# Optimization experiments

Hardware: AMD Instinct MI355X
Metric: run time of the kernel (lower is better)

The kernel has to match this reference:

```python
import jax, jax.numpy as jnp
import numpy as np

D_MODEL = 1024
D_STATE = 8
EXPAND = 2
EPS = 1e-5


def setup_inputs() -> dict:
    key = jax.random.key(0)
    ks = jax.random.split(key, 8)
    d_inner = D_MODEL * EXPAND
    x = jax.random.normal(ks[0], (2, 128, 196, D_MODEL), dtype=jnp.float32)
    # Linear params (torch convention: W [out, in], y = x @ W.T + b)
    W_proj = jax.random.normal(ks[1], (d_inner, D_MODEL), dtype=jnp.float32) * (1.0 / np.sqrt(D_MODEL))
    b_proj = jnp.zeros((d_inner,), dtype=jnp.float32)
    W_state = jax.random.normal(ks[2], (D_STATE, d_inner), dtype=jnp.float32) * (1.0 / np.sqrt(d_inner))
    b_state = jnp.zeros((D_STATE,), dtype=jnp.float32)
    W_out = jax.random.normal(ks[3], (D_MODEL, D_STATE), dtype=jnp.float32) * (1.0 / np.sqrt(D_STATE))
    b_out = jnp.zeros((D_MODEL,), dtype=jnp.float32)
    initial_state = jnp.zeros((1, D_STATE), dtype=jnp.float32)
    gamma = jnp.ones((D_MODEL,), dtype=jnp.float32)
    beta = jnp.zeros((D_MODEL,), dtype=jnp.float32)
    return {
        "x": x,
        "W_proj": W_proj, "b_proj": b_proj,
        "W_state": W_state, "b_state": b_state,
        "W_out": W_out, "b_out": b_out,
        "initial_state": initial_state,
        "gamma": gamma, "beta": beta,
    }


def reference(x, W_proj, b_proj, W_state, b_state, W_out, b_out, initial_state, gamma, beta):
    # The torch module loops over seq_len, but every step reads the fixed
    # initial_state (no recurrence) -> fully vectorized over all dims.
    # LayerNorm over d_model (eps=1e-5, torch default)
    mu = jnp.mean(x, axis=-1, keepdims=True)
    var = jnp.mean(jnp.square(x - mu), axis=-1, keepdims=True)
    xn = (x - mu) * jax.lax.rsqrt(var + EPS) * gamma + beta
    # proj: [b, s, p, d_model] -> [b, s, p, d_inner], then SiLU
    proj = jax.nn.silu(jnp.einsum('bspd,ed->bspe', xn, W_proj) + b_proj)
    # state projection: -> [b, s, p, d_state]
    state_updates = jnp.einsum('bspe,ne->bspn', proj, W_state) + b_state
    # initial_state [1, d_state] broadcast-added, then SiLU
    current_state = jax.nn.silu(initial_state.reshape(1, 1, 1, D_STATE) + state_updates)
    # out projection: -> [b, s, p, d_model]; dropout=0 (eval mode)
    out = jnp.einsum('bspn,dn->bspd', current_state, W_out) + b_out
    return x + out
```

## Files before the change

kernel.cpp:

```cpp
#include <hip/hip_runtime.h>
#include <hip/hip_bf16.h>

typedef unsigned short u16;
typedef unsigned int u32;
typedef __attribute__((ext_vector_type(8))) short bf16x8;
typedef __attribute__((ext_vector_type(4))) short bf16x4;
typedef __attribute__((ext_vector_type(4))) float f32x4;

#define T_TOKENS 50176
#define D_MODEL  1024
#define D_INNER  2048
#define D_STATE  8

__device__ __forceinline__ u16 f2bf(float f) {
    u32 u = __builtin_bit_cast(u32, f);
    u += 0x7fffu + ((u >> 16) & 1u);
    return (u16)(u >> 16);
}
__device__ __forceinline__ float bf2f(u16 h) {
    u32 u = ((u32)h) << 16;
    return __builtin_bit_cast(float, u);
}
__device__ __forceinline__ float silu(float v) {
    return v / (1.f + __expf(-v));
}

__device__ __forceinline__ f32x4 mfma_16x16x16_bf16(bf16x4 a, bf16x4 b, f32x4 c) {
#if __has_builtin(__builtin_amdgcn_mfma_f32_16x16x16bf16_1k)
    return __builtin_amdgcn_mfma_f32_16x16x16bf16_1k(a, b, c, 0, 0, 0);
#else
    f32x4 d;
    asm("v_mfma_f32_16x16x16_bf16 %0, %1, %2, %3" : "=v"(d) : "v"(a), "v"(b), "v"(c));
    return d;
#endif
}

__global__ __launch_bounds__(256) void k_ln(const float* __restrict__ x,
                                            const float* __restrict__ gamma,
                                            const float* __restrict__ beta,
                                            u16* __restrict__ xn) {
    const int w = threadIdx.x >> 6, lane = threadIdx.x & 63;
    const int tok = blockIdx.x * 4 + w;
    const float* xr = x + (size_t)tok * D_MODEL;
    float4 v[4];
    float s1 = 0.f, s2 = 0.f;
#pragma unroll
    for (int c = 0; c < 4; ++c) {
        v[c] = *(const float4*)(xr + c * 256 + lane * 4);
        s1 += v[c].x + v[c].y + v[c].z + v[c].w;
        s2 += v[c].x * v[c].x + v[c].y * v[c].y + v[c].z * v[c].z + v[c].w * v[c].w;
    }
#pragma unroll
    for (int off = 32; off; off >>= 1) {
        s1 += __shfl_xor(s1, off, 64);
        s2 += __shfl_xor(s2, off, 64);
    }
    const float mu = s1 * (1.f / 1024.f);
    const float var = s2 * (1.f / 1024.f) - mu * mu;
    const float rstd = rsqrtf(var + 1e-5f);
    u16* orow = xn + (size_t)tok * D_MODEL;
#pragma unroll
    for (int c = 0; c < 4; ++c) {
        const int d = c * 256 + lane * 4;
        float4 g = *(const float4*)(gamma + d);
        float4 b = *(const float4*)(beta + d);
        ushort4 o;
        o.x = f2bf((v[c].x - mu) * rstd * g.x + b.x);
        o.y = f2bf((v[c].y - mu) * rstd * g.y + b.y);
        o.z = f2bf((v[c].z - mu) * rstd * g.z + b.z);
        o.w = f2bf((v[c].w - mu) * rstd * g.w + b.w);
        *(ushort4*)(orow + d) = o;
    }
}

__global__ __launch_bounds__(256) void k_cvt(const float* __restrict__ W, u16* __restrict__ Wb) {
    const int i = (blockIdx.x * 256 + threadIdx.x) * 4;
    float4 v = *(const float4*)(W + i);
    ushort4 o = {f2bf(v.x), f2bf(v.y), f2bf(v.z), f2bf(v.w)};
    *(ushort4*)(Wb + i) = o;
}

__global__ __launch_bounds__(256) void k_gemm(const u16* __restrict__ A,
                                              const u16* __restrict__ B,
                                              const float* __restrict__ bproj,
                                              const float* __restrict__ Wstate,
                                              float* __restrict__ part) {
    __shared__ u16 As[128 * 64];
    __shared__ u16 Bs[128 * 64];
    const int t = threadIdx.x;
    const int w = t >> 6, lane = t & 63;
    const int q = lane >> 4, c15 = lane & 15;
    const int bn = blockIdx.x, bm = blockIdx.y;
    const int wm = (w >> 1) * 64, wn = (w & 1) * 64;

    f32x4 acc[4][4];
#pragma unroll
    for (int ci = 0; ci < 4; ++ci)
#pragma unroll
        for (int ti = 0; ti < 4; ++ti) acc[ci][ti] = (f32x4){0.f, 0.f, 0.f, 0.f};

    const int srow = t >> 3;
    const int sch = (t & 7) ^ (srow & 7);
    const u16* Ag = A + (size_t)(bm * 128 + srow) * 1024 + sch * 8;
    const u16* Bg = B + (size_t)(bn * 128 + srow) * 1024 + sch * 8;
    u16* lA = &As[t * 8];
    u16* lB = &Bs[t * 8];

    for (int kb = 0; kb < 16; ++kb) {
        __syncthreads();
#pragma unroll
        for (int i = 0; i < 4; ++i) {
            __builtin_amdgcn_global_load_lds(
                (const __attribute__((address_space(1))) void*)(Ag + (size_t)i * 32 * 1024 + kb * 64),
                (__attribute__((address_space(3))) void*)(lA + i * 2048), 16, 0, 0);
            __builtin_amdgcn_global_load_lds(
                (const __attribute__((address_space(1))) void*)(Bg + (size_t)i * 32 * 1024 + kb * 64),
                (__attribute__((address_space(3))) void*)(lB + i * 2048), 16, 0, 0);
        }
        __syncthreads();
#pragma unroll
        for (int ks = 0; ks < 2; ++ks) {
            bf16x8 xf[4], wf[4];
            const int chb = (ks * 4 + q) ^ (c15 & 7);
#pragma unroll
            for (int ti = 0; ti < 4; ++ti)
                xf[ti] = *(const bf16x8*)&As[(wm + ti * 16 + c15) * 64 + chb * 8];
#pragma unroll
            for (int ci = 0; ci < 4; ++ci)
                wf[ci] = *(const bf16x8*)&Bs[(wn + ci * 16 + c15) * 64 + chb * 8];
#pragma unroll
            for (int ci = 0; ci < 4; ++ci)
#pragma unroll
                for (int ti = 0; ti < 4; ++ti)
                    acc[ci][ti] = __builtin_amdgcn_mfma_f32_16x16x32_bf16(wf[ci], xf[ti], acc[ci][ti], 0, 0, 0);
        }
    }

    const int ib0 = bn * 128 + wn + q * 4;
    f32x4 bp4[4];
    bf16x4 wsf[4];
#pragma unroll
    for (int ci = 0; ci < 4; ++ci) {
        const int ib = ib0 + ci * 16;
        bp4[ci] = *(const f32x4*)(bproj + ib);
        if (c15 < 8) {
            f32x4 wv = *(const f32x4*)(Wstate + (size_t)c15 * D_INNER + ib);
            wsf[ci] = (bf16x4){(short)f2bf(wv[0]), (short)f2bf(wv[1]), (short)f2bf(wv[2]), (short)f2bf(wv[3])};
        } else {
            wsf[ci] = (bf16x4){0, 0, 0, 0};
        }
    }
    const int slot = bn * 2 + (w & 1);
#pragma unroll
    for (int ti = 0; ti < 4; ++ti) {
        f32x4 a2 = (f32x4){0.f, 0.f, 0.f, 0.f};
#pragma unroll
        for (int ci = 0; ci < 4; ++ci) {
            bf16x4 sv;
#pragma unroll
            for (int r = 0; r < 4; ++r) {
                const float s = silu(acc[ci][ti][r] + bp4[ci][r]);
                sv[r] = (short)f2bf(s);
            }
            a2 = mfma_16x16x16_bf16(wsf[ci], sv, a2);
        }
        if (q < 2) {
            const int row = bm * 128 + wm + ti * 16 + c15;
            *(f32x4*)(part + (size_t)row * 256 + slot * 8 + q * 4) = a2;
        }
    }
}

__global__ __launch_bounds__(256) void k_out2(const float* __restrict__ x,
                                              const float* __restrict__ part,
                                              const float* __restrict__ Wout,
                                              const float* __restrict__ bout,
                                              const float* __restrict__ bstate,
                                              const float* __restrict__ s0,
                                              float* __restrict__ out) {
    __shared__ float4 wol[2048];
    const int t = threadIdx.x;
    const float4* Wg4 = (const float4*)Wout;
#pragma unroll
    for (int i = 0; i < 8; ++i) {
        const int g = i * 256 + t;
        const int d = g >> 1;
        wol[g ^ ((d >> 2) & 7)] = Wg4[g];
    }
    __syncthreads();

    const int w = t >> 6, lane = t & 63;
    const int tok = blockIdx.x * 4 + w;

    const float4* p4 = (const float4*)(part + (size_t)tok * 256);
    float4 pv = p4[lane];
    float pa[4] = {pv.x, pv.y, pv.z, pv.w};
#pragma unroll
    for (int off = 2; off < 64; off <<= 1)
#pragma unroll
        for (int j = 0; j < 4; ++j) pa[j] += __shfl_xor(pa[j], off, 64);
    float cs[8];
#pragma unroll
    for (int j = 0; j < 4; ++j) {
        const float sl = __shfl(pa[j], 0, 64);
        const float sh = __shfl(pa[j], 1, 64);
        cs[j]     = silu(sl + s0[j]     + bstate[j]);
        cs[4 + j] = silu(sh + s0[4 + j] + bstate[4 + j]);
    }

    const float* xr = x + (size_t)tok * D_MODEL;
    float* orow = out + (size_t)tok * D_MODEL;
#pragma unroll
    for (int c = 0; c < 16; ++c) {
        const int d = c * 64 + lane;
        const int m = (d >> 2) & 7;
        const float4 w0 = wol[(d * 2) ^ m];
        const float4 w1 = wol[(d * 2 + 1) ^ m];
        float a = xr[d] + bout[d];
        a += cs[0] * w0.x + cs[1] * w0.y + cs[2] * w0.z + cs[3] * w0.w;
        a += cs[4] * w1.x + cs[5] * w1.y + cs[6] * w1.z + cs[7] * w1.w;
        orow[d] = a;
    }
}

extern "C" void kernel_launch(void* const* d_in, const int* in_sizes, int n_in,
                              void* d_out, int out_size, void* d_ws, size_t ws_size,
                              hipStream_t stream) {
    const float* x      = (const float*)d_in[0];
    const float* Wproj  = (const float*)d_in[1];
    const float* bproj  = (const float*)d_in[2];
    const float* Wstate = (const float*)d_in[3];
    const float* bstate = (const float*)d_in[4];
    const float* Wout   = (const float*)d_in[5];
    const float* bout   = (const float*)d_in[6];
    const float* s0     = (const float*)d_in[7];
    const float* gamma  = (const float*)d_in[8];
    const float* beta   = (const float*)d_in[9];

    u16* xn = (u16*)d_out;
    u16* Wb = (u16*)d_ws;
    float* partials = (float*)((char*)d_ws + (size_t)D_INNER * D_MODEL * sizeof(u16));
    float* out = (float*)d_out;

    k_ln  <<<T_TOKENS / 4, 256, 0, stream>>>(x, gamma, beta, xn);
    k_cvt <<<(D_INNER * D_MODEL) / 1024, 256, 0, stream>>>(Wproj, Wb);
    k_gemm<<<dim3(D_INNER / 128, T_TOKENS / 128), 256, 0, stream>>>(xn, Wb, bproj, Wstate, partials);
    k_out2<<<T_TOKENS / 4, 256, 0, stream>>>(x, partials, Wout, bout, bstate, s0, out);
}
```

Measured before the change: 745.3 us.

## Enlarge GEMM tile to 256x256 with double-buffered LDS pipeline

Result: faster. 692.6 us (-7.1%).

```diff
diff --git a/kernel.cpp b/kernel.cpp
--- a/kernel.cpp
+++ b/kernel.cpp
@@ -16,10 +16,6 @@
     u32 u = __builtin_bit_cast(u32, f);
     u += 0x7fffu + ((u >> 16) & 1u);
     return (u16)(u >> 16);
-}
-__device__ __forceinline__ float bf2f(u16 h) {
-    u32 u = ((u32)h) << 16;
-    return __builtin_bit_cast(float, u);
 }
 __device__ __forceinline__ float silu(float v) {
     return v / (1.f + __expf(-v));
@@ -80,63 +76,132 @@
     *(ushort4*)(Wb + i) = o;
 }
 
-__global__ __launch_bounds__(256) void k_gemm(const u16* __restrict__ A,
-                                              const u16* __restrict__ B,
-                                              const float* __restrict__ bproj,
-                                              const float* __restrict__ Wstate,
-                                              float* __restrict__ part) {
-    __shared__ u16 As[128 * 64];
-    __shared__ u16 Bs[128 * 64];
+#define STAGE_A(i, kb, buf) \
+    __builtin_amdgcn_global_load_lds( \
+        (const __attribute__((address_space(1))) void*)(Ag + (i) * 65536 + (kb) * 64), \
+        (__attribute__((address_space(3))) void*)(lA + (buf) * 32768 + (i) * 4096), 16, 0, 0)
+#define STAGE_B(i, kb, buf) \
+    __builtin_amdgcn_global_load_lds( \
+        (const __attribute__((address_space(1))) void*)(Bg + (i) * 65536 + (kb) * 64), \
+        (__attribute__((address_space(3))) void*)(lB + (buf) * 32768 + (i) * 4096), 16, 0, 0)
+#define FENCE() asm volatile("" ::: "memory")
+#define BARRIER() do { FENCE(); __builtin_amdgcn_s_barrier(); FENCE(); } while (0)
+
+__global__ __launch_bounds__(512, 2) void k_gemm(const u16* __restrict__ A,
+                                                 const u16* __restrict__ B,
+                                                 const float* __restrict__ bproj,
+                                                 const float* __restrict__ Wstate,
+                                                 float* __restrict__ part) {
+    __shared__ u16 sm[65536];
     const int t = threadIdx.x;
     const int w = t >> 6, lane = t & 63;
     const int q = lane >> 4, c15 = lane & 15;
     const int bn = blockIdx.x, bm = blockIdx.y;
-    const int wm = (w >> 1) * 64, wn = (w & 1) * 64;
-
-    f32x4 acc[4][4];
+    const int wm = (w >> 2) * 128, wn = (w & 3) * 64;
+
+    f32x4 acc[4][8];
 #pragma unroll
     for (int ci = 0; ci < 4; ++ci)
 #pragma unroll
-        for (int ti = 0; ti < 4; ++ti) acc[ci][ti] = (f32x4){0.f, 0.f, 0.f, 0.f};
+        for (int ti = 0; ti < 8; ++ti) acc[ci][ti] = (f32x4){0.f, 0.f, 0.f, 0.f};
 
     const int srow = t >> 3;
-    const int sch = (t & 7) ^ (srow & 7);
-    const u16* Ag = A + (size_t)(bm * 128 + srow) * 1024 + sch * 8;
-    const u16* Bg = B + (size_t)(bn * 128 + srow) * 1024 + sch * 8;
-    u16* lA = &As[t * 8];
-    u16* lB = &Bs[t * 8];
-
-    for (int kb = 0; kb < 16; ++kb) {
-        __syncthreads();
-#pragma unroll
-        for (int i = 0; i < 4; ++i) {
-            __builtin_amdgcn_global_load_lds(
-                (const __attribute__((address_space(1))) void*)(Ag + (size_t)i * 32 * 1024 + kb * 64),
-                (__attribute__((address_space(3))) void*)(lA + i * 2048), 16, 0, 0);
-            __builtin_amdgcn_global_load_lds(
-                (const __attribute__((address_space(1))) void*)(Bg + (size_t)i * 32 * 1024 + kb * 64),
-                (__attribute__((address_space(3))) void*)(lB + i * 2048), 16, 0, 0);
-        }
-        __syncthreads();
-#pragma unroll
-        for (int ks = 0; ks < 2; ++ks) {
-            bf16x8 xf[4], wf[4];
-            const int chb = (ks * 4 + q) ^ (c15 & 7);
+    const int gch = (t & 7) ^ (srow & 7);
+    const u16* Ag = A + (size_t)(bm * 256 + srow) * 1024 + gch * 8;
+    const u16* Bg = B + (size_t)(bn * 256 + srow) * 1024 + gch * 8;
+    u16* lA = &sm[t * 8];
+    u16* lB = &sm[16384 + t * 8];
+
+    auto LDA = [&](int buf, int ti, int ks) -> bf16x8 {
+        const int row = wm + ti * 16 + c15;
+        const int ch = (ks * 4 + q) ^ (c15 & 7);
+        return *(const bf16x8*)&sm[buf * 32768 + row * 64 + ch * 8];
+    };
+    auto LDB = [&](int buf, int ci, int ks) -> bf16x8 {
+        const int row = wn + ci * 16 + c15;
+        const int ch = (ks * 4 + q) ^ (c15 & 7);
+        return *(const bf16x8*)&sm[buf * 32768 + 16384 + row * 64 + ch * 8];
+    };
+
+    STAGE_A(0, 0, 0); STAGE_A(1, 0, 0); STAGE_A(2, 0, 0); STAGE_A(3, 0, 0);
+    STAGE_B(0, 0, 0); STAGE_B(1, 0, 0); STAGE_B(2, 0, 0); STAGE_B(3, 0, 0);
+    STAGE_A(0, 1, 1); STAGE_A(1, 1, 1);
+    asm volatile("s_waitcnt vmcnt(2)" ::: "memory");
+    BARRIER();
+
+#pragma unroll 2
+    for (int tt = 0; tt < 16; ++tt) {
+        const int cur = tt & 1, nxt = cur ^ 1;
+        const int kb1 = (tt + 1) & 15, kb2 = (tt + 2) & 15;
+        bf16x8 xf[4][2], wf[4][2];
+#pragma unroll
+        for (int ti = 0; ti < 4; ++ti)
+#pragma unroll
+            for (int ks = 0; ks < 2; ++ks) xf[ti][ks] = LDA(cur, ti, ks);
+#pragma unroll
+        for (int ci = 0; ci < 2; ++ci)
+#pragma unroll
+            for (int ks = 0; ks < 2; ++ks) wf[ci][ks] = LDB(cur, ci, ks);
+        STAGE_A(2, kb1, nxt); STAGE_A(3, kb1, nxt);
+        BARRIER();
+        __builtin_amdgcn_s_setprio(1);
+#pragma unroll
+        for (int ci = 0; ci < 2; ++ci)
 #pragma unroll
             for (int ti = 0; ti < 4; ++ti)
-                xf[ti] = *(const bf16x8*)&As[(wm + ti * 16 + c15) * 64 + chb * 8];
-#pragma unroll
-            for (int ci = 0; ci < 4; ++ci)
-                wf[ci] = *(const bf16x8*)&Bs[(wn + ci * 16 + c15) * 64 + chb * 8];
-#pragma unroll
-            for (int ci = 0; ci < 4; ++ci)
-#pragma unroll
-                for (int ti = 0; ti < 4; ++ti)
-                    acc[ci][ti] = __builtin_amdgcn_mfma_f32_16x16x32_bf16(wf[ci], xf[ti], acc[ci][ti], 0, 0, 0);
-        }
-    }
-
-    const int ib0 = bn * 128 + wn + q * 4;
+#pragma unroll
+                for (int ks = 0; ks < 2; ++ks)
+                    acc[ci][ti] = __builtin_amdgcn_mfma_f32_16x16x32_bf16(wf[ci][ks], xf[ti][ks], acc[ci][ti], 0, 0, 0);
+        __builtin_amdgcn_s_setprio(0);
+        BARRIER();
+#pragma unroll
+        for (int ci = 2; ci < 4; ++ci)
+#pragma unroll
+            for (int ks = 0; ks < 2; ++ks) wf[ci][ks] = LDB(cur, ci, ks);
+        STAGE_B(0, kb1, nxt); STAGE_B(1, kb1, nxt);
+        BARRIER();
+        __builtin_amdgcn_s_setprio(1);
+#pragma unroll
+        for (int ci = 2; ci < 4; ++ci)
+#pragma unroll
+            for (int ti = 0; ti < 4; ++ti)
+#pragma unroll
+                for (int ks = 0; ks < 2; ++ks)
+                    acc[ci][ti] = __builtin_amdgcn_mfma_f32_16x16x32_bf16(wf[ci][ks], xf[ti][ks], acc[ci][ti], 0, 0, 0);
+        __builtin_amdgcn_s_setprio(0);
+        BARRIER();
+#pragma unroll
+        for (int ti = 0; ti < 4; ++ti)
+#pragma unroll
+            for (int ks = 0; ks < 2; ++ks) xf[ti][ks] = LDA(cur, 4 + ti, ks);
+        STAGE_B(2, kb1, nxt); STAGE_B(3, kb1, nxt);
+        BARRIER();
+        __builtin_amdgcn_s_setprio(1);
+#pragma unroll
+        for (int ci = 0; ci < 2; ++ci)
+#pragma unroll
+            for (int ti = 0; ti < 4; ++ti)
+#pragma unroll
+                for (int ks = 0; ks < 2; ++ks)
+                    acc[ci][4 + ti] = __builtin_amdgcn_mfma_f32_16x16x32_bf16(wf[ci][ks], xf[ti][ks], acc[ci][4 + ti], 0, 0, 0);
+        __builtin_amdgcn_s_setprio(0);
+        BARRIER();
+        STAGE_A(0, kb2, cur); STAGE_A(1, kb2, cur);
+        asm volatile("s_waitcnt vmcnt(2)" ::: "memory");
+        BARRIER();
+        __builtin_amdgcn_s_setprio(1);
+#pragma unroll
+        for (int ci = 2; ci < 4; ++ci)
+#pragma unroll
+            for (int ti = 0; ti < 4; ++ti)
+#pragma unroll
+                for (int ks = 0; ks < 2; ++ks)
+                    acc[ci][4 + ti] = __builtin_amdgcn_mfma_f32_16x16x32_bf16(wf[ci][ks], xf[ti][ks], acc[ci][4 + ti], 0, 0, 0);
+        __builtin_amdgcn_s_setprio(0);
+        BARRIER();
+    }
+
+    const int ib0 = bn * 256 + wn + q * 4;
     f32x4 bp4[4];
     bf16x4 wsf[4];
 #pragma unroll
@@ -150,9 +215,9 @@
             wsf[ci] = (bf16x4){0, 0, 0, 0};
         }
     }
-    const int slot = bn * 2 + (w & 1);
-#pragma unroll
-    for (int ti = 0; ti < 4; ++ti) {
+    const int slot = bn * 4 + (w & 3);
+#pragma unroll
+    for (int ti = 0; ti < 8; ++ti) {
         f32x4 a2 = (f32x4){0.f, 0.f, 0.f, 0.f};
 #pragma unroll
         for (int ci = 0; ci < 4; ++ci) {
@@ -165,7 +230,7 @@
             a2 = mfma_16x16x16_bf16(wsf[ci], sv, a2);
         }
         if (q < 2) {
-            const int row = bm * 128 + wm + ti * 16 + c15;
+            const int row = bm * 256 + wm + ti * 16 + c15;
             *(f32x4*)(part + (size_t)row * 256 + slot * 8 + q * 4) = a2;
         }
     }
@@ -244,6 +309,6 @@
 
     k_ln  <<<T_TOKENS / 4, 256, 0, stream>>>(x, gamma, beta, xn);
     k_cvt <<<(D_INNER * D_MODEL) / 1024, 256, 0, stream>>>(Wproj, Wb);
-    k_gemm<<<dim3(D_INNER / 128, T_TOKENS / 128), 256, 0, stream>>>(xn, Wb, bproj, Wstate, partials);
+    k_gemm<<<dim3(D_INNER / 256, T_TOKENS / 256), 512, 0, stream>>>(xn, Wb, bproj, Wstate, partials);
     k_out2<<<T_TOKENS / 4, 256, 0, stream>>>(x, partials, Wout, bout, bstate, s0, out);
 }
```
